# Kernel tuning notes

Hardware: AMD Instinct MI355X
Metric: run time of the kernel (lower is better)

The kernel has to match this reference:

```python
import jax, jax.numpy as jnp
import numpy as np
from functools import partial

EPS = 1e-5
TOP_K = 1
NUM_EXPERTS = 3
LOSS_COEF = 0.01


def conv2d(x, w, stride, pad):
    return jax.lax.conv_general_dilated(
        x, w, (stride, stride), [(pad, pad), (pad, pad)],
        dimension_numbers=("NCHW", "OIHW", "NCHW"))


def setup_inputs() -> dict:
    key = jax.random.key(0)
    ks = jax.random.split(key, 8)
    b, c, t, h, w = 8, 3, 5, 512, 512
    E = NUM_EXPERTS
    s = 0.05  # small init scale
    return {
        "x": jax.random.normal(ks[0], (b, c, t, h, w), jnp.float32),
        "g_conv_w": jax.random.normal(ks[1], (64, 15, 7, 7), jnp.float32) * s,
        "g_bn_gamma": jnp.ones((64,), jnp.float32),
        "g_bn_beta": jnp.zeros((64,), jnp.float32),
        "g_bn_mean": jnp.zeros((64,), jnp.float32),
        "g_bn_var": jnp.ones((64,), jnp.float32),
        "g_fc_w": jax.random.normal(ks[2], (E, 64), jnp.float32) * s,
        "g_fc_b": jnp.zeros((E,), jnp.float32),
        "e_conv1_w": jax.random.normal(ks[3], (E, 64, 15, 7, 7), jnp.float32) * s,
        "e_conv2_w": jax.random.normal(ks[4], (E, 128, 64, 3, 3), jnp.float32) * s,
        "e_head_w1": jax.random.normal(ks[5], (E, 128, 128, 3, 3), jnp.float32) * s,
        "e_head_b1": jnp.zeros((E, 128), jnp.float32),
        "e_head_w2": jax.random.normal(ks[6], (E, 5, 128, 1, 1), jnp.float32) * s,
        "e_head_b2": jnp.zeros((E, 5), jnp.float32),
    }


def gating(xr, g_conv_w, g_bn_gamma, g_bn_beta, g_bn_mean, g_bn_var, g_fc_w, g_fc_b):
    # backbone: conv 7x7 s2 -> BN (eval) -> ReLU -> maxpool 3x3 s2 -> GAP -> fc
    f = conv2d(xr, g_conv_w, 2, 3)
    scale = g_bn_gamma / jnp.sqrt(g_bn_var + EPS)
    f = f * scale[None, :, None, None] + (g_bn_beta - g_bn_mean * scale)[None, :, None, None]
    f = jax.nn.relu(f)
    f = jax.lax.reduce_window(f, -jnp.inf, jax.lax.max, (1, 1, 3, 3), (1, 1, 2, 2),
                              [(0, 0), (0, 0), (1, 1), (1, 1)])
    pooled = f.mean(axis=(2, 3))                       # (b, 64)
    logits = pooled @ g_fc_w.T + g_fc_b                # (b, E)
    b = logits.shape[0]
    _, top_idx = jax.lax.top_k(logits, TOP_K)          # (b, k)
    rows = jnp.arange(b)[:, None]
    # eval-mode gating: uniform 1/k over selected experts
    sparse_gates = jnp.zeros_like(logits).at[rows, top_idx].set(1.0 / TOP_K)
    expert_mask = jnp.zeros_like(logits).at[rows, top_idx].set(1.0)
    density = expert_mask.mean(axis=0)
    density_proxy = jax.nn.softmax(logits, axis=1).mean(axis=0)
    aux_loss = (density * density_proxy).sum() * NUM_EXPERTS
    return sparse_gates, aux_loss


def expert_forward(xr, w1, w2, hw1, hb1, hw2, hb2):
    y = jax.nn.relu(conv2d(xr, w1, 2, 3))              # (b, 64, H/2, W/2)
    y = jax.nn.relu(conv2d(y, w2, 2, 1))               # (b, 128, H/4, W/4)
    y = jax.nn.relu(conv2d(y, hw1, 1, 1) + hb1[None, :, None, None])
    y = conv2d(y, hw2, 1, 0) + hb2[None, :, None, None]  # (b, 5, H/4, W/4)
    return y


def reference(x, g_conv_w, g_bn_gamma, g_bn_beta, g_bn_mean, g_bn_var, g_fc_w, g_fc_b,
              e_conv1_w, e_conv2_w, e_head_w1, e_head_b1, e_head_w2, e_head_b2):
    b, c, t, h, w = x.shape
    xr = x.reshape(b, c * t, h, w)
    sparse_gates, aux_loss = gating(xr, g_conv_w, g_bn_gamma, g_bn_beta,
                                    g_bn_mean, g_bn_var, g_fc_w, g_fc_b)
    # run all experts (gates are 0 for unselected -> identical math to sparse dispatch)
    outs = jax.vmap(lambda w1, w2, hw1, hb1, hw2, hb2:
                    expert_forward(xr, w1, w2, hw1, hb1, hw2, hb2))(
        e_conv1_w, e_conv2_w, e_head_w1, e_head_b1, e_head_w2, e_head_b2)  # (E,b,5,h4,w4)
    combined = jnp.einsum("ebchw,be->bchw", outs, sparse_gates)
    hm, wh, reg = combined[:, 0:1], combined[:, 1:3], combined[:, 3:5]
    return hm, wh, reg, LOSS_COEF * aux_loss
```

## Files before the change

kernel.cpp:

```cpp
#include <hip/hip_runtime.h>
#include <cstdint>
#include <cmath>


typedef _Float16 f16x8 __attribute__((ext_vector_type(8)));
typedef _Float16 f16x4 __attribute__((ext_vector_type(4)));
typedef float f32x4 __attribute__((ext_vector_type(4)));

__device__ __forceinline__ void g2l16(const void* g, void* l) {
  __builtin_amdgcn_global_load_lds((__attribute__((address_space(1))) void*)g,
                                   (__attribute__((address_space(3))) void*)l,
                                   16, 0, 0);
}

__device__ __forceinline__ int xcd_swz(int bid, int nwg) {
  return (bid & 7) * (nwg >> 3) + (bid >> 3);
}

__global__ __launch_bounds__(256) void prep_x_k(
    const float* __restrict__ x, _Float16* __restrict__ xp)
{
  const int t = blockIdx.x * 256 + threadIdx.x;
  const int pix = t & 262143;
  const int b   = t >> 18;
  const float* src = x + (size_t)b * 15 * 262144 + pix;
  f16x8 lo, hi;
#pragma unroll
  for (int c = 0; c < 8; ++c)  lo[c] = (_Float16)src[(size_t)c * 262144];
#pragma unroll
  for (int c = 8; c < 15; ++c) hi[c - 8] = (_Float16)src[(size_t)c * 262144];
  hi[7] = (_Float16)0.f;
  *(f16x8*)&xp[(size_t)t * 16]     = lo;
  *(f16x8*)&xp[(size_t)t * 16 + 8] = hi;
}

__global__ __launch_bounds__(256) void prep_w7_k(
    const float* __restrict__ gw, const float* __restrict__ ew,
    _Float16* __restrict__ wp)
{
  const int i = blockIdx.x * 256 + threadIdx.x;
  const int kk   = i & 31;
  const int cout = (i >> 5) & 63;
  const int pair = (i >> 11) & 3;
  const int v    = i >> 13;
  const int ky = v % 7, set = v / 7;
  const int t = kk >> 4, cin = kk & 15;
  const int kx = 2 * pair + t;
  float val = 0.f;
  if (cin < 15 && kx < 7) {
    if (set == 0) val = gw[((cout * 15 + cin) * 7 + ky) * 7 + kx];
    else          val = ew[((((set - 1) * 64 + cout) * 15 + cin) * 7 + ky) * 7 + kx];
  }
  wp[i] = (_Float16)val;
}

template<int CINC>
__global__ __launch_bounds__(256) void prep_w3_k(
    const float* __restrict__ w, _Float16* __restrict__ wp)
{
  constexpr int CH = CINC / 32;
  const int i = blockIdx.x * 256 + threadIdx.x;
  const int kk   = i & 31;
  const int cout = (i >> 5) & 127;
  int rest = i >> 12;
  const int ch  = rest % CH;  rest /= CH;
  const int tap = rest % 9;
  const int e   = rest / 9;
  const int cin = ch * 32 + kk;
  wp[i] = (_Float16)w[((size_t)(e * 128 + cout) * CINC + cin) * 9 + tap];
}

template<int MODE, int SWZ>
__global__ __launch_bounds__(256, 3) void conv7m_k(
    const _Float16* __restrict__ xp, const _Float16* __restrict__ wp,
    const float* __restrict__ bn_g, const float* __restrict__ bn_b,
    const float* __restrict__ bn_m, const float* __restrict__ bn_v,
    const int* __restrict__ sel, _Float16* __restrict__ out)
{
  constexpr int ROWF = 518 * 16;
  __shared__ __align__(16) _Float16 smem[18432];
  const int sb = SWZ ? xcd_swz(blockIdx.x, 2048) : (int)blockIdx.x;
  const int oy = sb & 255, b = sb >> 8;
  const int wv = threadIdx.x >> 6, lane = threadIdx.x & 63;
  const int ln15 = lane & 15, quad = lane >> 4;
  const int npx0 = wv * 64;

  int set = 0;
  if constexpr (MODE == 1) set = 1 + sel[b];
  const _Float16* wset = wp + (size_t)set * (7 * 4 * 64 * 32);
  const _Float16* xb   = xp + (size_t)b * (512 * 512 * 16);

  const _Float16* xrow[7];
  bool rowok[7];
#pragma unroll
  for (int ky = 0; ky < 7; ++ky) {
    const int iy = 2 * oy - 3 + ky;
    rowok[ky] = (unsigned)iy < 512u;
    const int iyc = iy < 0 ? 0 : (iy > 511 ? 511 : iy);
    xrow[ky] = xb + (size_t)iyc * (512 * 16);
  }

  if (threadIdx.x < 32) {
    const int bi = threadIdx.x >> 4, k = threadIdx.x & 15;
    if (k < 12) {
      const int g = (k < 6) ? k : (1030 + k - 6);
      f16x8 z = {};
      *(f16x8*)&smem[bi * ROWF + g * 8] = z;
    }
  }

  f32x4 acc[4][4];
#pragma unroll
  for (int f = 0; f < 4; ++f)
#pragma unroll
    for (int g = 0; g < 4; ++g) acc[f][g] = (f32x4){0.f, 0.f, 0.f, 0.f};

  auto load_af = [&](int t, f16x8* af) {
    const int ky = t >> 2, pair = t & 3;
    const _Float16* wt = wset + (size_t)((ky * 4 + pair) * 64) * 32;
#pragma unroll
    for (int f = 0; f < 4; ++f)
      af[f] = *(const f16x8*)&wt[(f * 16 + ln15) * 32 + quad * 8];
  };
  auto stage = [&](int ky, int bi) {
    _Float16* bufb = &smem[bi * ROWF];
    const _Float16* xr = xrow[ky];
#pragma unroll
    for (int s = 0; s < 4; ++s) {
      const int seg = wv * 4 + s;
      const int gl = 6 + seg * 64 + lane;
      const int gs = gl ^ ((gl >> 3) & 7);
      g2l16(xr + (size_t)((gs >> 1) - 3) * 16 + (gs & 1) * 8,
            bufb + (6 + seg * 64) * 8);
    }
  };

  int gb[4];
#pragma unroll
  for (int g = 0; g < 4; ++g)
    gb[g] = 4 * (npx0 + g * 16 + ln15) + quad;

  f16x8 afA[4], afB[4];
  load_af(0, afA);
  stage(0, 0);
  __syncthreads();

#pragma unroll
  for (int t = 0; t < 28; ++t) {
    const int ky = t >> 2, pair = t & 3;
    const int cur = ky & 1;
    f16x8* afc = (t & 1) ? afB : afA;
    f16x8* afn = (t & 1) ? afA : afB;
    if (t + 1 < 28) load_af(t + 1, afn);
    if (pair == 0 && ky + 1 < 7) stage(ky + 1, cur ^ 1);
    if (rowok[ky]) {
      const _Float16* bufb = &smem[cur * ROWF];
#pragma unroll
      for (int g = 0; g < 4; ++g) {
        const int gq = gb[g] + 4 * pair;
        const int gs = gq ^ ((gq >> 3) & 7);
        const f16x8 bf = *(const f16x8*)&bufb[gs * 8];
#pragma unroll
        for (int f = 0; f < 4; ++f)
          acc[f][g] = __builtin_amdgcn_mfma_f32_16x16x32_f16(afc[f], bf, acc[f][g], 0, 0, 0);
      }
    }
    if (pair == 3) __syncthreads();
  }

  _Float16* sw = &smem[wv * 4608];
#pragma unroll
  for (int f = 0; f < 4; ++f) {
    float scl[4], add[4];
#pragma unroll
    for (int r = 0; r < 4; ++r) {
      const int cout = f * 16 + quad * 4 + r;
      if constexpr (MODE == 0) {
        const float sc = bn_g[cout] * rsqrtf(bn_v[cout] + 1e-5f);
        scl[r] = sc; add[r] = bn_b[cout] - bn_m[cout] * sc;
      } else { scl[r] = 1.f; add[r] = 0.f; }
    }
#pragma unroll
    for (int g = 0; g < 4; ++g) {
      f16x4 h;
#pragma unroll
      for (int r = 0; r < 4; ++r)
        h[r] = (_Float16)fmaxf(acc[f][g][r] * scl[r] + add[r], 0.f);
      *(f16x4*)&sw[(g * 16 + ln15) * 72 + f * 16 + quad * 4] = h;
    }
  }
  __syncthreads();
  const size_t rowbase = ((size_t)(b * 256 + oy) * 256 + npx0) * 64;
#pragma unroll
  for (int i = 0; i < 8; ++i) {
    const int pxl = (lane >> 3) + i * 8;
    const int c8  = (lane & 7) * 8;
    const f16x8 v = *(const f16x8*)&sw[pxl * 72 + c8];
    *(f16x8*)&out[rowbase + (size_t)pxl * 64 + c8] = v;
  }
}

template<int CINC, int S, int INSZ, int OUTSZ, int MODE>
__global__ __launch_bounds__(256, 3) void conv3m_k(
    const _Float16* __restrict__ xp, const _Float16* __restrict__ wp,
    const float* __restrict__ p_bias, const int* __restrict__ sel,
    _Float16* __restrict__ out)
{
  constexpr int CH  = CINC / 32;
  constexpr int NCH = 3 * CH;
  constexpr int NT  = NCH * 3;
  constexpr int NPX = (S == 1) ? (OUTSZ + 2) : (2 * OUTSZ + 1);
  constexpr int ROWF = NPX * 32;
  constexpr int NGR  = NPX * 4;
  constexpr int SPW  = INSZ / 64;
  constexpr int SMEMF = (4 * ROWF > 18432) ? 4 * ROWF : 18432;
  __shared__ __align__(16) _Float16 smem[SMEMF];
  const int sb = xcd_swz(blockIdx.x, OUTSZ * 8);
  const int oy = sb % OUTSZ, b = sb / OUTSZ;
  const int wv = threadIdx.x >> 6, lane = threadIdx.x & 63;
  const int ln15 = lane & 15, quad = lane >> 4;
  const int mwb = (wv >> 1) * 64, nwb = (wv & 1) * 64;

  const int e = sel[b];
  const _Float16* we = wp + (size_t)e * (9 * CH * 128 * 32);
  const _Float16* xb = xp + (size_t)b * ((size_t)INSZ * INSZ * CINC);

  const _Float16* xrow[3];
  bool rowok[3];
#pragma unroll
  for (int ky = 0; ky < 3; ++ky) {
    const int iy = S * oy + ky - 1;
    rowok[ky] = (unsigned)iy < (unsigned)INSZ;
    const int iyc = iy < 0 ? 0 : (iy >= INSZ ? INSZ - 1 : iy);
    xrow[ky] = xb + (size_t)iyc * INSZ * CINC;
  }

  {
    constexpr int HGPB = (S == 1) ? 8 : 4;
    if (threadIdx.x < 4 * HGPB) {
      const int bi = threadIdx.x / HGPB, k = threadIdx.x % HGPB;
      const int g = (k < 4) ? k : (NGR - 8 + k);
      f16x8 z = {};
      *(f16x8*)&smem[bi * ROWF + g * 8] = z;
    }
  }

  f32x4 acc[4][4];
#pragma unroll
  for (int f = 0; f < 4; ++f)
#pragma unroll
    for (int g = 0; g < 4; ++g) acc[f][g] = (f32x4){0.f, 0.f, 0.f, 0.f};

  auto load_af = [&](int t, f16x8* af) {
    const int c = t / 3, kx = t % 3;
    const int ky = c / CH, ch = c % CH;
    const _Float16* wt = we + (size_t)(((ky * 3 + kx) * CH + ch) * 128) * 32;
#pragma unroll
    for (int f = 0; f < 4; ++f)
      af[f] = *(const f16x8*)&wt[(mwb + f * 16 + ln15) * 32 + quad * 8];
  };
  auto stage = [&](int c, int bi) {
    const int ky = c / CH, ch = c % CH;
    _Float16* bufb = &smem[bi * ROWF];
    const _Float16* xr = xrow[ky];
#pragma unroll
    for (int s = 0; s < SPW; ++s) {
      const int seg = wv * SPW + s;
      const int gl = 4 + seg * 64 + lane;
      const int gs = gl ^ ((gl >> 3) & 7);
      g2l16(xr + (size_t)((gs >> 2) - 1) * CINC + ch * 32 + (gs & 3) * 8,
            bufb + (4 + seg * 64) * 8);
    }
  };

  int gb[4];
#pragma unroll
  for (int g = 0; g < 4; ++g) {
    const int ox = nwb + g * 16 + ln15;
    gb[g] = 4 * S * ox + quad;
  }

  f16x8 afb[3][4];
  load_af(0, afb[0]);
  load_af(1, afb[1]);
  stage(0, 0);
  stage(1, 1);
  __syncthreads();

#pragma unroll
  for (int t = 0; t < NT; ++t) {
    const int c = t / 3, kx = t % 3;
    const int ky = c / CH;
    const int cur = c & 3;
    if (t + 2 < NT) load_af(t + 2, afb[(t + 2) % 3]);
    if (kx == 0 && (c & 1) == 0) {
      if (c + 2 < NCH) stage(c + 2, (c + 2) & 3);
      if (c + 3 < NCH) stage(c + 3, (c + 3) & 3);
    }
    if (rowok[ky]) {
      const _Float16* bufb = &smem[cur * ROWF];
#pragma unroll
      for (int g = 0; g < 4; ++g) {
        const int gq = gb[g] + 4 * kx;
        const int gs = gq ^ ((gq >> 3) & 7);
        const f16x8 bf = *(const f16x8*)&bufb[gs * 8];
#pragma unroll
        for (int f = 0; f < 4; ++f)
          acc[f][g] = __builtin_amdgcn_mfma_f32_16x16x32_f16(afb[t % 3][f], bf, acc[f][g], 0, 0, 0);
      }
    }
    if (kx == 2 && (c & 1)) __syncthreads();
  }

  _Float16* sw = &smem[wv * 4608];
#pragma unroll
  for (int f = 0; f < 4; ++f) {
#pragma unroll
    for (int g = 0; g < 4; ++g) {
      f16x4 h;
#pragma unroll
      for (int r = 0; r < 4; ++r) {
        const int cout = mwb + f * 16 + quad * 4 + r;
        float v = acc[f][g][r];
        if constexpr (MODE == 2) v += p_bias[e * 128 + cout];
        h[r] = (_Float16)fmaxf(v, 0.f);
      }
      *(f16x4*)&sw[(g * 16 + ln15) * 72 + f * 16 + quad * 4] = h;
    }
  }
  __syncthreads();
  const size_t rowbase = ((size_t)(b * OUTSZ + oy) * OUTSZ + nwb) * 128 + mwb;
#pragma unroll
  for (int i = 0; i < 8; ++i) {
    const int pxl = (lane >> 3) + i * 8;
    const int c8  = (lane & 7) * 8;
    const f16x8 v = *(const f16x8*)&sw[pxl * 72 + c8];
    *(f16x8*)&out[rowbase + (size_t)pxl * 128 + c8] = v;
  }
}

__global__ void zero_k(float* __restrict__ pooled) {
  if (threadIdx.x < 512) pooled[threadIdx.x] = 0.f;
}

__global__ __launch_bounds__(256) void pool_k(
    const _Float16* __restrict__ f, float* __restrict__ pooled)
{
  const int sb = xcd_swz(blockIdx.x, 1024);
  const int b  = sb >> 7;
  const int py = sb & 127;
  const int wv = threadIdx.x >> 6, lane = threadIdx.x & 63;
  const int c8  = (lane & 7) * 8;
  const int pxq = lane >> 3;
  const _Float16* fb = f + (size_t)b * 256 * 256 * 64;

  const int y0 = 2 * py - 1;
  float s[8];
#pragma unroll
  for (int j = 0; j < 8; ++j) s[j] = 0.f;

#pragma unroll
  for (int step = 0; step < 4; ++step) {
    const int px = wv * 32 + step * 8 + pxq;
    const int x0 = 2 * px - 1;
    f16x8 m;
#pragma unroll
    for (int j = 0; j < 8; ++j) m[j] = (_Float16)(-60000.f);
#pragma unroll
    for (int dy = 0; dy < 3; ++dy) {
      const int y = y0 + dy;
      if ((unsigned)y < 256u) {
        const _Float16* row = fb + (size_t)y * 256 * 64 + c8;
        if (x0 >= 0)
          m = __builtin_elementwise_max(m, *(const f16x8*)&row[(size_t)x0 * 64]);
        m = __builtin_elementwise_max(m, *(const f16x8*)&row[(size_t)(x0 + 1) * 64]);
        m = __builtin_elementwise_max(m, *(const f16x8*)&row[(size_t)(x0 + 2) * 64]);
      }
    }
#pragma unroll
    for (int j = 0; j < 8; ++j) s[j] += (float)m[j];
  }

  __shared__ float red[256][8];
#pragma unroll
  for (int j = 0; j < 8; ++j) red[threadIdx.x][j] = s[j];
  __syncthreads();
  if (threadIdx.x < 64) {
    const int c = threadIdx.x, cg = c >> 3, cj = c & 7;
    float t = 0.f;
#pragma unroll
    for (int k = 0; k < 32; ++k)
      t += red[(k >> 3) * 64 + (k & 7) * 8 + cg][cj];
    atomicAdd(&pooled[b * 64 + c], t);
  }
}

__global__ __launch_bounds__(64) void gate_k(
    const float* __restrict__ pooled, const float* __restrict__ fcw,
    const float* __restrict__ fcb, int* __restrict__ sel, float* __restrict__ out_aux)
{
  __shared__ float probs[8][3];
  __shared__ int sidx[8];
  const int b = threadIdx.x;
  if (b < 8) {
    float l[3];
#pragma unroll
    for (int e = 0; e < 3; ++e) {
      float s = fcb[e];
      for (int c = 0; c < 64; ++c)
        s = fmaf(pooled[b * 64 + c] * (1.f / 16384.f), fcw[e * 64 + c], s);
      l[e] = s;
    }
    int best = 0;
    if (l[1] > l[best]) best = 1;
    if (l[2] > l[best]) best = 2;
    sel[b] = best;
    sidx[b] = best;
    const float m = fmaxf(l[0], fmaxf(l[1], l[2]));
    const float e0 = expf(l[0] - m), e1 = expf(l[1] - m), e2 = expf(l[2] - m);
    const float inv = 1.f / (e0 + e1 + e2);
    probs[b][0] = e0 * inv; probs[b][1] = e1 * inv; probs[b][2] = e2 * inv;
  }
  __syncthreads();
  if (threadIdx.x == 0) {
    float cnt[3] = {0.f, 0.f, 0.f}, pr[3] = {0.f, 0.f, 0.f};
    for (int bb = 0; bb < 8; ++bb) {
      cnt[sidx[bb]] += 1.f;
#pragma unroll
      for (int e = 0; e < 3; ++e) pr[e] += probs[bb][e];
    }
    float aux = 0.f;
#pragma unroll
    for (int e = 0; e < 3; ++e) aux += (cnt[e] * 0.125f) * (pr[e] * 0.125f);
    *out_aux = 0.01f * (3.f * aux);
  }
}

__global__ __launch_bounds__(256) void head2m_k(
    const _Float16* __restrict__ in, const float* __restrict__ w,
    const float* __restrict__ b2, const int* __restrict__ sel,
    float* __restrict__ out)
{
  const int b = blockIdx.x >> 6;
  const int p = ((blockIdx.x & 63) << 8) + threadIdx.x;
  const int e = sel[b];
  const float* wp = w + (size_t)e * 5 * 128;
  const _Float16* ip = in + ((size_t)(b << 14) + p) * 128;
  float a0 = 0.f, a1 = 0.f, a2 = 0.f, a3 = 0.f, a4 = 0.f;
#pragma unroll
  for (int cc = 0; cc < 16; ++cc) {
    const f16x8 v8 = *(const f16x8*)&ip[cc * 8];
#pragma unroll
    for (int j = 0; j < 8; ++j) {
      const float v = (float)v8[j];
      const int c = cc * 8 + j;
      a0 = fmaf(v, wp[c], a0);
      a1 = fmaf(v, wp[128 + c], a1);
      a2 = fmaf(v, wp[256 + c], a2);
      a3 = fmaf(v, wp[384 + c], a3);
      a4 = fmaf(v, wp[512 + c], a4);
    }
  }
  a0 += b2[e * 5 + 0]; a1 += b2[e * 5 + 1]; a2 += b2[e * 5 + 2];
  a3 += b2[e * 5 + 3]; a4 += b2[e * 5 + 4];
  out[(b << 14) + p] = a0;
  out[131072 + ((b * 2 + 0) << 14) + p] = a1;
  out[131072 + ((b * 2 + 1) << 14) + p] = a2;
  out[393216 + ((b * 2 + 0) << 14) + p] = a3;
  out[393216 + ((b * 2 + 1) << 14) + p] = a4;
}

extern "C" void kernel_launch(void* const* d_in, const int* in_sizes, int n_in,
                              void* d_out, int out_size, void* d_ws, size_t ws_size,
                              hipStream_t stream) {
  const float* x          = (const float*)d_in[0];
  const float* g_conv_w   = (const float*)d_in[1];
  const float* g_bn_gamma = (const float*)d_in[2];
  const float* g_bn_beta  = (const float*)d_in[3];
  const float* g_bn_mean  = (const float*)d_in[4];
  const float* g_bn_var   = (const float*)d_in[5];
  const float* g_fc_w     = (const float*)d_in[6];
  const float* g_fc_b     = (const float*)d_in[7];
  const float* e_conv1_w  = (const float*)d_in[8];
  const float* e_conv2_w  = (const float*)d_in[9];
  const float* e_head_w1  = (const float*)d_in[10];
  const float* e_head_b1  = (const float*)d_in[11];
  const float* e_head_w2  = (const float*)d_in[12];
  const float* e_head_b2  = (const float*)d_in[13];
  float* out = (float*)d_out;

  _Float16* xp      = (_Float16*)d_ws;
  _Float16* featbuf = xp + 33554432;
  _Float16* y2      = featbuf + 33554432;
  _Float16* w7p     = y2 + 16777216;
  _Float16* w2p     = w7p + 229376;
  _Float16* w3p     = w2p + 221184;
  _Float16* y3      = xp;
  float*    pooled  = (float*)(w3p + 442368);
  int*      sel     = (int*)(pooled + 512);

  prep_x_k<<<8192, 256, 0, stream>>>(x, xp);
  prep_w7_k<<<896, 256, 0, stream>>>(g_conv_w, e_conv1_w, w7p);
  prep_w3_k<64><<<864, 256, 0, stream>>>(e_conv2_w, w2p);
  prep_w3_k<128><<<1728, 256, 0, stream>>>(e_head_w1, w3p);
  zero_k<<<1, 512, 0, stream>>>(pooled);

  conv7m_k<0, 1><<<2048, 256, 0, stream>>>(xp, w7p, g_bn_gamma, g_bn_beta,
                                           g_bn_mean, g_bn_var, nullptr, featbuf);
  pool_k<<<1024, 256, 0, stream>>>(featbuf, pooled);
  gate_k<<<1, 64, 0, stream>>>(pooled, g_fc_w, g_fc_b, sel, out + 655360);

  conv7m_k<1, 1><<<2048, 256, 0, stream>>>(xp, w7p, nullptr, nullptr, nullptr, nullptr,
                                           sel, featbuf);
  conv3m_k<64, 2, 256, 128, 1><<<1024, 256, 0, stream>>>(featbuf, w2p, nullptr, sel, y2);
  conv3m_k<128, 1, 128, 128, 2><<<1024, 256, 0, stream>>>(y2, w3p, e_head_b1, sel, y3);
  head2m_k<<<512, 256, 0, stream>>>(y3, e_head_w2, e_head_b2, sel, out);
}
```

Measured before the change: 473.3 us.

## Vectorize input repack through LDS and raise wave priority around MFMA loops

The input repack kernel now has each thread read float4 vectors from every channel plane, convert them to half, and stage the results in swizzled shared memory. It then writes out coalesced 16-half pixel records, with four pixels per thread and a quarter as many blocks as before. Separately, s_setprio raises wave priority around the MFMA inner loops of the 7x7 and 3x3 conv kernels so that matrix work gets scheduled ahead of the load phases of other waves. The costs are extra shared memory and a barrier in the prep kernel, and the priority hints may not help.

```diff
diff --git a/kernel.cpp b/kernel.cpp
--- a/kernel.cpp
+++ b/kernel.cpp
@@ -20,18 +20,48 @@
 __global__ __launch_bounds__(256) void prep_x_k(
     const float* __restrict__ x, _Float16* __restrict__ xp)
 {
-  const int t = blockIdx.x * 256 + threadIdx.x;
-  const int pix = t & 262143;
-  const int b   = t >> 18;
-  const float* src = x + (size_t)b * 15 * 262144 + pix;
-  f16x8 lo, hi;
-#pragma unroll
-  for (int c = 0; c < 8; ++c)  lo[c] = (_Float16)src[(size_t)c * 262144];
-#pragma unroll
-  for (int c = 8; c < 15; ++c) hi[c - 8] = (_Float16)src[(size_t)c * 262144];
-  hi[7] = (_Float16)0.f;
-  *(f16x8*)&xp[(size_t)t * 16]     = lo;
-  *(f16x8*)&xp[(size_t)t * 16 + 8] = hi;
+  __shared__ __align__(16) _Float16 st[16384];
+  const int tid = threadIdx.x;
+  const int b   = blockIdx.x >> 8;
+  const int blk = blockIdx.x & 255;
+  const int px0 = blk * 1024;
+  const float* src = x + (size_t)b * 15 * 262144 + px0 + tid * 4;
+
+  f16x8 lo[4], hi[4];
+#pragma unroll
+  for (int j = 0; j < 4; ++j) hi[j][7] = (_Float16)0.f;
+#pragma unroll
+  for (int c = 0; c < 15; ++c) {
+    const float4 v = *(const float4*)&src[(size_t)c * 262144];
+    if (c < 8) {
+      lo[0][c] = (_Float16)v.x; lo[1][c] = (_Float16)v.y;
+      lo[2][c] = (_Float16)v.z; lo[3][c] = (_Float16)v.w;
+    } else {
+      hi[0][c - 8] = (_Float16)v.x; hi[1][c - 8] = (_Float16)v.y;
+      hi[2][c - 8] = (_Float16)v.z; hi[3][c - 8] = (_Float16)v.w;
+    }
+  }
+#pragma unroll
+  for (int j = 0; j < 4; ++j) {
+#pragma unroll
+    for (int h = 0; h < 2; ++h) {
+      const int g  = (tid * 4 + j) * 2 + h;
+      const int gs = g ^ ((g >> 3) & 7);
+      *(f16x8*)&st[gs * 8] = h ? hi[j] : lo[j];
+    }
+  }
+  __syncthreads();
+  _Float16* dst = xp + ((size_t)b * 262144 + px0) * 16;
+#pragma unroll
+  for (int m = 0; m < 4; ++m) {
+    const int px = m * 256 + tid;
+#pragma unroll
+    for (int h = 0; h < 2; ++h) {
+      const int g  = px * 2 + h;
+      const int gs = g ^ ((g >> 3) & 7);
+      *(f16x8*)&dst[(size_t)px * 16 + h * 8] = *(const f16x8*)&st[gs * 8];
+    }
+  }
 }
 
 __global__ __launch_bounds__(256) void prep_w7_k(
@@ -155,6 +185,7 @@
     if (pair == 0 && ky + 1 < 7) stage(ky + 1, cur ^ 1);
     if (rowok[ky]) {
       const _Float16* bufb = &smem[cur * ROWF];
+      __builtin_amdgcn_s_setprio(1);
 #pragma unroll
       for (int g = 0; g < 4; ++g) {
         const int gq = gb[g] + 4 * pair;
@@ -164,6 +195,7 @@
         for (int f = 0; f < 4; ++f)
           acc[f][g] = __builtin_amdgcn_mfma_f32_16x16x32_f16(afc[f], bf, acc[f][g], 0, 0, 0);
       }
+      __builtin_amdgcn_s_setprio(0);
     }
     if (pair == 3) __syncthreads();
   }
@@ -299,6 +331,7 @@
     }
     if (rowok[ky]) {
       const _Float16* bufb = &smem[cur * ROWF];
+      __builtin_amdgcn_s_setprio(1);
 #pragma unroll
       for (int g = 0; g < 4; ++g) {
         const int gq = gb[g] + 4 * kx;
@@ -308,6 +341,7 @@
         for (int f = 0; f < 4; ++f)
           acc[f][g] = __builtin_amdgcn_mfma_f32_16x16x32_f16(afb[t % 3][f], bf, acc[f][g], 0, 0, 0);
       }
+      __builtin_amdgcn_s_setprio(0);
     }
     if (kx == 2 && (c & 1)) __syncthreads();
   }
@@ -499,7 +533,7 @@
   float*    pooled  = (float*)(w3p + 442368);
   int*      sel     = (int*)(pooled + 512);
 
-  prep_x_k<<<8192, 256, 0, stream>>>(x, xp);
+  prep_x_k<<<2048, 256, 0, stream>>>(x, xp);
   prep_w7_k<<<896, 256, 0, stream>>>(g_conv_w, e_conv1_w, w7p);
   prep_w3_k<64><<<864, 256, 0, stream>>>(e_conv2_w, w2p);
   prep_w3_k<128><<<1728, 256, 0, stream>>>(e_head_w1, w3p);
```

Result: no change. 473.1 us (-0.0%).
